# Kernel optimization log

Hardware: AMD Instinct MI355X
Metric: run time of the kernel (lower is better)

The kernel has to match this reference:

```python
import jax, jax.numpy as jnp
import numpy as np

D_MODEL = 1024
N_HEAD = 16
STRIDE = 1024
SEQ = STRIDE + 1  # time_mask is (stride+1, stride+1) -> N must equal stride+1
BATCH = 4
EPS = 1e-5


def layer_norm(x, g, b):
    mu = jnp.mean(x, axis=-1, keepdims=True)
    var = jnp.var(x, axis=-1, keepdims=True)
    return (x - mu) * jax.lax.rsqrt(var + EPS) * g + b


def quick_gelu(x):
    return x * jax.nn.sigmoid(1.702 * x)


def setup_inputs() -> dict:
    key = jax.random.key(0)
    ks = jax.random.split(key, 12)
    C = D_MODEL
    s = 0.02
    return {
        "x": jax.random.normal(ks[0], (SEQ, BATCH, C), dtype=jnp.float32),
        "qkv_w": jax.random.normal(ks[1], (3 * C, C), dtype=jnp.float32) * s,
        "proj_w": jax.random.normal(ks[2], (C, C), dtype=jnp.float32) * s,
        "proj_b": jnp.zeros((C,), dtype=jnp.float32),
        "ln1_g": jnp.ones((C,), dtype=jnp.float32),
        "ln1_b": jnp.zeros((C,), dtype=jnp.float32),
        "ln2_g": jnp.ones((C,), dtype=jnp.float32),
        "ln2_b": jnp.zeros((C,), dtype=jnp.float32),
        "fc_w": jax.random.normal(ks[3], (4 * C, C), dtype=jnp.float32) * s,
        "fc_b": jnp.zeros((4 * C,), dtype=jnp.float32),
        "cproj_w": jax.random.normal(ks[4], (C, 4 * C), dtype=jnp.float32) * s,
        "cproj_b": jnp.zeros((C,), dtype=jnp.float32),
    }


def _attention(xs, qkv_w, proj_w, proj_b):
    # xs: [N, B, C] (seq-first) -> internal [B, N, C]
    xb = jnp.transpose(xs, (1, 0, 2))
    B, N, C = xb.shape
    H, Dh = N_HEAD, C // N_HEAD
    scale = Dh ** -0.5
    qkv = xb @ qkv_w.T  # [B, N, 3C], no bias (qkv_bias=False)
    qkv = qkv.reshape(B, N, 3, H, Dh).transpose(2, 0, 3, 1, 4)  # [3, B, H, N, Dh]
    q, k, v = qkv[0], qkv[1], qkv[2]
    attn = jnp.einsum("bhnd,bhmd->bhnm", q, k) * scale
    mask = jnp.tril(jnp.ones((N, N), dtype=bool))  # time_mask: causal tril
    attn = jnp.where(mask, attn, -jnp.inf)
    attn = jax.nn.softmax(attn, axis=-1)
    out = jnp.einsum("bhnm,bhmd->bhnd", attn, v)  # [B, H, N, Dh]
    out = out.transpose(0, 2, 1, 3).reshape(B, N, C)
    out = out @ proj_w.T + proj_b
    return jnp.transpose(out, (1, 0, 2)), attn  # back to [N, B, C]


def reference(x, qkv_w, proj_w, proj_b, ln1_g, ln1_b, ln2_g, ln2_b,
              fc_w, fc_b, cproj_w, cproj_b):
    y, attn = _attention(layer_norm(x, ln1_g, ln1_b), qkv_w, proj_w, proj_b)
    x = x + y
    h = layer_norm(x, ln2_g, ln2_b)
    h = quick_gelu(h @ fc_w.T + fc_b) @ cproj_w.T + cproj_b
    x = x + h
    return (x, attn)
```

## Files before the change

### kernel.cpp

```cpp
#include <hip/hip_runtime.h>


typedef unsigned short ushort_t;
typedef __bf16 bf16x8 __attribute__((ext_vector_type(8)));
typedef float f32x4 __attribute__((ext_vector_type(4)));

#define SEQ_N   1025
#define CMODEL  1024
#define NHEAD   16
#define DH      64
#define TTOK    4100
#define MP      4224
#define NPAD    1152
#define BH      64

__device__ __forceinline__ ushort_t f2bf(float f) {
  union { float f; unsigned u; } v; v.f = f;
  unsigned r = v.u + 0x7fffu + ((v.u >> 16) & 1u);
  return (ushort_t)(r >> 16);
}

__device__ __forceinline__ void gl_lds16(const void* g, void* s) {
  __builtin_amdgcn_global_load_lds(
      (const __attribute__((address_space(1))) unsigned int*)g,
      (__attribute__((address_space(3))) unsigned int*)s, 16, 0, 0);
}

__global__ void cvt_bf(const float* __restrict__ src, ushort_t* __restrict__ dst, int n) {
  int i = (blockIdx.x * 256 + threadIdx.x) * 4;
  if (i >= n) return;
  float4 f = *(const float4*)(src + i);
  dst[i + 0] = f2bf(f.x);
  dst[i + 1] = f2bf(f.y);
  dst[i + 2] = f2bf(f.z);
  dst[i + 3] = f2bf(f.w);
}

__global__ __launch_bounds__(256)
void ln_bf(const float* __restrict__ xin, const float* __restrict__ g,
           const float* __restrict__ bb, ushort_t* __restrict__ out) {
  const int t = blockIdx.x;
  const float* row = xin + (size_t)t * CMODEL;
  const int base = threadIdx.x * 4;
  const float4 v = *(const float4*)(row + base);
  float s = v.x + v.y + v.z + v.w;
  float q = v.x * v.x + v.y * v.y + v.z * v.z + v.w * v.w;
#pragma unroll
  for (int off = 32; off > 0; off >>= 1) {
    s += __shfl_down(s, off);
    q += __shfl_down(q, off);
  }
  __shared__ float sh[8];
  const int wave = threadIdx.x >> 6, lane = threadIdx.x & 63;
  if (lane == 0) { sh[wave] = s; sh[4 + wave] = q; }
  __syncthreads();
  if (threadIdx.x == 0) {
    const float ts = sh[0] + sh[1] + sh[2] + sh[3];
    const float tq = sh[4] + sh[5] + sh[6] + sh[7];
    const float mean = ts * (1.f / CMODEL);
    const float var = tq * (1.f / CMODEL) - mean * mean;
    sh[0] = mean; sh[1] = rsqrtf(var + 1e-5f);
  }
  __syncthreads();
  const float mean = sh[0], rstd = sh[1];
  const float4 gg = *(const float4*)(g + base);
  const float4 bv = *(const float4*)(bb + base);
  ushort_t* orow = out + (size_t)t * CMODEL;
  orow[base + 0] = f2bf((v.x - mean) * rstd * gg.x + bv.x);
  orow[base + 1] = f2bf((v.y - mean) * rstd * gg.y + bv.y);
  orow[base + 2] = f2bf((v.z - mean) * rstd * gg.z + bv.z);
  orow[base + 3] = f2bf((v.w - mean) * rstd * gg.w + bv.w);
}

template <int EPI>
__global__ __launch_bounds__(256)
void gemm_bt(const ushort_t* __restrict__ A, int lda,
             const ushort_t* __restrict__ B, int ldb,
             int K,
             const float* __restrict__ bias, const float* __restrict__ res,
             float* __restrict__ outf, ushort_t* __restrict__ outb,
             ushort_t* __restrict__ oq, ushort_t* __restrict__ ok,
             ushort_t* __restrict__ ovt) {
  __shared__ __align__(16) ushort_t lsA[128 * 32];
  __shared__ __align__(16) ushort_t lsB[128 * 32];
  const int tid = threadIdx.x;
  const int wave = tid >> 6, lane = tid & 63;
  const int lr = lane & 15, quad = lane >> 4;
  const int tM = blockIdx.y * 128, tN = blockIdx.x * 128;
  const int waveM = (wave >> 1) * 64, waveN = (wave & 1) * 64;

  f32x4 acc[4][4];
  const f32x4 z4 = {0.f, 0.f, 0.f, 0.f};
#pragma unroll
  for (int i = 0; i < 4; ++i)
#pragma unroll
    for (int j = 0; j < 4; ++j) acc[i][j] = z4;

  for (int k0 = 0; k0 < K; k0 += 32) {
    __syncthreads();
#pragma unroll
    for (int p = 0; p < 2; ++p) {
      const int idx = p * 256 + wave * 64 + lane;
      const int row = idx >> 2, part = idx & 3;
      const int cb = (p * 256 + wave * 64) * 8;
      gl_lds16(A + (size_t)(tM + row) * lda + k0 + part * 8, lsA + cb);
      gl_lds16(B + (size_t)(tN + row) * ldb + k0 + part * 8, lsB + cb);
    }
    __syncthreads();
    bf16x8 af[4], bfr[4];
#pragma unroll
    for (int mi = 0; mi < 4; ++mi)
      af[mi] = *(const bf16x8*)(lsA + (waveM + mi * 16 + lr) * 32 + quad * 8);
#pragma unroll
    for (int ni = 0; ni < 4; ++ni)
      bfr[ni] = *(const bf16x8*)(lsB + (waveN + ni * 16 + lr) * 32 + quad * 8);
#pragma unroll
    for (int mi = 0; mi < 4; ++mi)
#pragma unroll
      for (int ni = 0; ni < 4; ++ni)
        acc[mi][ni] = __builtin_amdgcn_mfma_f32_16x16x32_bf16(af[mi], bfr[ni], acc[mi][ni], 0, 0, 0);
  }

#pragma unroll
  for (int mi = 0; mi < 4; ++mi) {
#pragma unroll
    for (int ni = 0; ni < 4; ++ni) {
#pragma unroll
      for (int r = 0; r < 4; ++r) {
        const int m = tM + waveM + mi * 16 + quad * 4 + r;
        const int n = tN + waveN + ni * 16 + lr;
        const float v = acc[mi][ni][r];
        if constexpr (EPI == 0) {
          if (m < TTOK) {
            const int b_ = m & 3, ns = m >> 2;
            const int which = n >> 10, rem = n & 1023, h = rem >> 6, d = rem & 63;
            const int bh = b_ * NHEAD + h;
            const ushort_t bv = f2bf(v);
            if (which == 0)      oq[((size_t)bh * NPAD + ns) * DH + d] = bv;
            else if (which == 1) ok[((size_t)bh * NPAD + ns) * DH + d] = bv;
            else                 ovt[((size_t)bh * DH + d) * NPAD + ns] = bv;
          }
        } else if constexpr (EPI == 3) {
          if (m < TTOK)
            outf[(size_t)m * CMODEL + n] = v + bias[n] + res[(size_t)m * CMODEL + n];
        } else if constexpr (EPI == 4) {
          if (m < TTOK) {
            const float zv = v + bias[n];
            outb[(size_t)m * 4096 + n] = f2bf(zv / (1.f + __expf(-1.702f * zv)));
          }
        }
      }
    }
  }
}

__global__ __launch_bounds__(256)
void attn_fused(const ushort_t* __restrict__ qb, const ushort_t* __restrict__ kb,
                const ushort_t* __restrict__ vtb, float* __restrict__ attn,
                ushort_t* __restrict__ ao) {
  __shared__ __align__(16) char smem[34816 + 17408 + 512];
  ushort_t* lsK  = (ushort_t*)smem;
  ushort_t* lsP  = (ushort_t*)smem;
  float*    lpart = (float*)smem;
  ushort_t* lsQV = (ushort_t*)(smem + 34816);
  float*    linvs = (float*)(smem + 34816 + 17408);

  const int bh = blockIdx.x;
  const int iT = 8 - blockIdx.y;
  const int tM = iT * 128;
  const int tid = threadIdx.x;
  const int wave = tid >> 6, lane = tid & 63;
  const int lr = lane & 15, quad = lane >> 4;
  const int waveM = (wave >> 1) * 64, waveN = (wave & 1) * 64;

  const ushort_t* Qg = qb + (size_t)bh * NPAD * DH;
  const ushort_t* Kg = kb + (size_t)bh * NPAD * DH;
  const ushort_t* Vg = vtb + (size_t)bh * DH * NPAD;
  float* attn_h = attn + (size_t)bh * ((size_t)SEQ_N * SEQ_N);

#pragma unroll
  for (int p = 0; p < 4; ++p) {
    const int c = p * 256 + wave * 64 + lane;
    const int ks = c >> 9, n = (c >> 2) & 127, part = c & 3;
    gl_lds16(Qg + (size_t)(tM + n) * DH + ks * 32 + part * 8,
             lsQV + (size_t)(p * 256 + wave * 64) * 8);
  }
  __syncthreads();
  bf16x8 aq[4][2];
#pragma unroll
  for (int mi = 0; mi < 4; ++mi)
#pragma unroll
    for (int ks = 0; ks < 2; ++ks)
      aq[mi][ks] = *(const bf16x8*)(lsQV + ks * 4096 + (waveM + mi * 16 + lr) * 32 + quad * 8);
  __syncthreads();

  f32x4 acc[4][4];
  const f32x4 z4 = {0.f, 0.f, 0.f, 0.f};

  float lsum[4][4];
#pragma unroll
  for (int mi = 0; mi < 4; ++mi)
#pragma unroll
    for (int r = 0; r < 4; ++r) lsum[mi][r] = 0.f;

  for (int j = 0; j <= iT; ++j) {
    __syncthreads();
#pragma unroll
    for (int p = 0; p < 4; ++p) {
      const int c = p * 256 + wave * 64 + lane;
      const int ks = c >> 9, n = (c >> 2) & 127, part = c & 3;
      gl_lds16(Kg + (size_t)(j * 128 + n) * DH + ks * 32 + part * 8,
               lsK + (size_t)(p * 256 + wave * 64) * 8);
    }
    __syncthreads();
#pragma unroll
    for (int mi = 0; mi < 4; ++mi)
#pragma unroll
      for (int ni = 0; ni < 4; ++ni) acc[mi][ni] = z4;
#pragma unroll
    for (int ks = 0; ks < 2; ++ks) {
      bf16x8 bk[4];
#pragma unroll
      for (int ni = 0; ni < 4; ++ni)
        bk[ni] = *(const bf16x8*)(lsK + ks * 4096 + (waveN + ni * 16 + lr) * 32 + quad * 8);
#pragma unroll
      for (int mi = 0; mi < 4; ++mi)
#pragma unroll
        for (int ni = 0; ni < 4; ++ni)
          acc[mi][ni] = __builtin_amdgcn_mfma_f32_16x16x32_bf16(aq[mi][ks], bk[ni], acc[mi][ni], 0, 0, 0);
    }
#pragma unroll
    for (int mi = 0; mi < 4; ++mi)
#pragma unroll
      for (int ni = 0; ni < 4; ++ni)
#pragma unroll
        for (int r = 0; r < 4; ++r) {
          const int row = tM + waveM + mi * 16 + quad * 4 + r;
          const int col = j * 128 + waveN + ni * 16 + lr;
          if (col <= row) lsum[mi][r] += __expf(acc[mi][ni][r] * 0.125f);
        }
  }
#pragma unroll
  for (int mi = 0; mi < 4; ++mi)
#pragma unroll
    for (int r = 0; r < 4; ++r) {
      float s = lsum[mi][r];
      s += __shfl_xor(s, 1); s += __shfl_xor(s, 2);
      s += __shfl_xor(s, 4); s += __shfl_xor(s, 8);
      lsum[mi][r] = s;
    }
  __syncthreads();
  if (lr == 0) {
    const int wx = wave & 1;
#pragma unroll
    for (int mi = 0; mi < 4; ++mi)
#pragma unroll
      for (int r = 0; r < 4; ++r)
        lpart[wx * 128 + waveM + mi * 16 + quad * 4 + r] = lsum[mi][r];
  }
  __syncthreads();
  if (tid < 128) linvs[tid] = 1.0f / (lpart[tid] + lpart[128 + tid]);
  __syncthreads();
  float linv[4][4];
#pragma unroll
  for (int mi = 0; mi < 4; ++mi)
#pragma unroll
    for (int r = 0; r < 4; ++r)
      linv[mi][r] = linvs[waveM + mi * 16 + quad * 4 + r];

  f32x4 oacc[2][4];
#pragma unroll
  for (int i = 0; i < 2; ++i)
#pragma unroll
    for (int j = 0; j < 4; ++j) oacc[i][j] = z4;
  const int prow = wave * 32;
  const int wrow = wave * 32;
  const int lcol = lane;

  for (int j = 0; j <= iT; ++j) {
    __syncthreads();
#pragma unroll
    for (int p = 0; p < 4; ++p) {
      const int c = p * 256 + wave * 64 + lane;
      const int ks = c >> 9, n = (c >> 2) & 127, part = c & 3;
      gl_lds16(Kg + (size_t)(j * 128 + n) * DH + ks * 32 + part * 8,
               lsK + (size_t)(p * 256 + wave * 64) * 8);
    }
#pragma unroll
    for (int p = 0; p < 4; ++p) {
      const int c = p * 256 + tid;
      const int n = c >> 4, klc = c & 15;
      const uint4 v = *(const uint4*)(Vg + (size_t)n * NPAD + j * 128 + klc * 8);
      *(uint4*)(lsQV + (size_t)n * 136 + klc * 8) = v;
    }
    __syncthreads();
#pragma unroll
    for (int mi = 0; mi < 4; ++mi)
#pragma unroll
      for (int ni = 0; ni < 4; ++ni) acc[mi][ni] = z4;
#pragma unroll
    for (int ks = 0; ks < 2; ++ks) {
      bf16x8 bk[4];
#pragma unroll
      for (int ni = 0; ni < 4; ++ni)
        bk[ni] = *(const bf16x8*)(lsK + ks * 4096 + (waveN + ni * 16 + lr) * 32 + quad * 8);
#pragma unroll
      for (int mi = 0; mi < 4; ++mi)
#pragma unroll
        for (int ni = 0; ni < 4; ++ni)
          acc[mi][ni] = __builtin_amdgcn_mfma_f32_16x16x32_bf16(aq[mi][ks], bk[ni], acc[mi][ni], 0, 0, 0);
    }
    __syncthreads();
#pragma unroll
    for (int mi = 0; mi < 4; ++mi)
#pragma unroll
      for (int ni = 0; ni < 4; ++ni)
#pragma unroll
        for (int r = 0; r < 4; ++r) {
          const int rowl = waveM + mi * 16 + quad * 4 + r;
          const int coll = waveN + ni * 16 + lr;
          const int row = tM + rowl;
          const int col = j * 128 + coll;
          const float pv = (col <= row) ? __expf(acc[mi][ni][r] * 0.125f) * linv[mi][r] : 0.f;
          lsP[(size_t)rowl * 136 + coll] = f2bf(pv);
        }
    __syncthreads();
#pragma unroll
    for (int ks = 0; ks < 4; ++ks) {
      bf16x8 ap[2], bv[4];
#pragma unroll
      for (int mi2 = 0; mi2 < 2; ++mi2)
        ap[mi2] = *(const bf16x8*)(lsP + (size_t)(prow + mi2 * 16 + lr) * 136 + ks * 32 + quad * 8);
#pragma unroll
      for (int ni = 0; ni < 4; ++ni)
        bv[ni] = *(const bf16x8*)(lsQV + (size_t)(ni * 16 + lr) * 136 + ks * 32 + quad * 8);
#pragma unroll
      for (int mi2 = 0; mi2 < 2; ++mi2)
#pragma unroll
        for (int ni = 0; ni < 4; ++ni)
          oacc[mi2][ni] = __builtin_amdgcn_mfma_f32_16x16x32_bf16(ap[mi2], bv[ni], oacc[mi2][ni], 0, 0, 0);
    }
#pragma unroll 8
    for (int rr = 0; rr < 32; ++rr) {
      const int grow = tM + wrow + rr;
      if (grow >= SEQ_N) break;
      const ushort_t* lrow = lsP + (size_t)(wrow + rr) * 136;
#pragma unroll
      for (int cb = 0; cb < 2; ++cb) {
        const int gcol = j * 128 + cb * 64 + lcol;
        union { unsigned u; float f; } cv;
        cv.u = ((unsigned)lrow[cb * 64 + lcol]) << 16;
        if (gcol < SEQ_N)
          __builtin_nontemporal_store(cv.f, attn_h + (size_t)grow * SEQ_N + gcol);
      }
    }
  }

  const int b_ = bh >> 4, h = bh & 15;
#pragma unroll
  for (int mi2 = 0; mi2 < 2; ++mi2)
#pragma unroll
    for (int ni = 0; ni < 4; ++ni)
#pragma unroll
      for (int r = 0; r < 4; ++r) {
        const int row = tM + prow + mi2 * 16 + quad * 4 + r;
        const int d = ni * 16 + lr;
        if (row < SEQ_N)
          ao[((size_t)row * 4 + b_) * CMODEL + h * DH + d] = f2bf(oacc[mi2][ni][r]);
      }

  const int c0 = tM + 128;
  if (c0 <= 1024) {
    const int width = 1025 - c0;
    for (int r = wave; r < 128; r += 4) {
      float* rp = attn_h + (size_t)(tM + r) * SEQ_N + c0;
      int pre = ((16 - (int)(((uintptr_t)rp) & 15)) >> 2) & 3;
      if (pre > width) pre = width;
      for (int c = lane; c < pre; c += 64) rp[c] = 0.f;
      const int body = (width - pre) >> 2;
      f32x4* bp = (f32x4*)(rp + pre);
      const f32x4 zf4 = {0.f, 0.f, 0.f, 0.f};
      for (int c = lane; c < body; c += 64) __builtin_nontemporal_store(zf4, bp + c);
      for (int c = pre + body * 4 + lane; c < width; c += 64) rp[c] = 0.f;
    }
  }
}

extern "C" void kernel_launch(void* const* d_in, const int* in_sizes, int n_in,
                              void* d_out, int out_size, void* d_ws, size_t ws_size,
                              hipStream_t stream) {
  const float* x       = (const float*)d_in[0];
  const float* qkv_w   = (const float*)d_in[1];
  const float* proj_w  = (const float*)d_in[2];
  const float* proj_b  = (const float*)d_in[3];
  const float* ln1_g   = (const float*)d_in[4];
  const float* ln1_b   = (const float*)d_in[5];
  const float* ln2_g   = (const float*)d_in[6];
  const float* ln2_b   = (const float*)d_in[7];
  const float* fc_w    = (const float*)d_in[8];
  const float* fc_b    = (const float*)d_in[9];
  const float* cproj_w = (const float*)d_in[10];
  const float* cproj_b = (const float*)d_in[11];

  float* out_x = (float*)d_out;
  float* out_attn = out_x + (size_t)TTOK * CMODEL;

  char* p = (char*)d_ws;
  auto alloc = [&](size_t bytes) { char* r = p; p += (bytes + 255) & ~(size_t)255; return r; };
  ushort_t* ln1x  = (ushort_t*)alloc((size_t)MP * CMODEL * 2);
  ushort_t* wqkv  = (ushort_t*)alloc((size_t)3072 * 1024 * 2);
  ushort_t* wproj = (ushort_t*)alloc((size_t)1024 * 1024 * 2);
  ushort_t* wfc   = (ushort_t*)alloc((size_t)4096 * 1024 * 2);
  ushort_t* wcpr  = (ushort_t*)alloc((size_t)1024 * 4096 * 2);
  ushort_t* qb    = (ushort_t*)alloc((size_t)BH * NPAD * DH * 2);
  ushort_t* kb    = (ushort_t*)alloc((size_t)BH * NPAD * DH * 2);
  ushort_t* vtb   = (ushort_t*)alloc((size_t)BH * DH * NPAD * 2);
  ushort_t* aob   = (ushort_t*)alloc((size_t)MP * CMODEL * 2);
  float*    x1    = (float*)alloc((size_t)MP * CMODEL * 4);
  ushort_t* ln2x  = (ushort_t*)alloc((size_t)MP * CMODEL * 2);
  ushort_t* hb    = (ushort_t*)alloc((size_t)MP * 4096 * 2);
  (void)ws_size; (void)in_sizes; (void)n_in; (void)out_size;

  cvt_bf<<<3072, 256, 0, stream>>>(qkv_w, wqkv, 3072 * 1024);
  cvt_bf<<<1024, 256, 0, stream>>>(proj_w, wproj, 1024 * 1024);
  cvt_bf<<<4096, 256, 0, stream>>>(fc_w, wfc, 4096 * 1024);
  cvt_bf<<<4096, 256, 0, stream>>>(cproj_w, wcpr, 4096 * 1024);

  ln_bf<<<TTOK, 256, 0, stream>>>(x, ln1_g, ln1_b, ln1x);

  gemm_bt<0><<<dim3(24, 33, 1), 256, 0, stream>>>(ln1x, 1024, wqkv, 1024, 1024,
      nullptr, nullptr, nullptr, nullptr, qb, kb, vtb);

  attn_fused<<<dim3(64, 9), 256, 0, stream>>>(qb, kb, vtb, out_attn, aob);

  gemm_bt<3><<<dim3(8, 33, 1), 256, 0, stream>>>(aob, 1024, wproj, 1024, 1024,
      proj_b, x, x1, nullptr, nullptr, nullptr, nullptr);

  ln_bf<<<TTOK, 256, 0, stream>>>(x1, ln2_g, ln2_b, ln2x);

  gemm_bt<4><<<dim3(32, 33, 1), 256, 0, stream>>>(ln2x, 1024, wfc, 1024, 1024,
      fc_b, nullptr, nullptr, hb, nullptr, nullptr, nullptr);

  gemm_bt<3><<<dim3(8, 33, 1), 256, 0, stream>>>(hb, 4096, wcpr, 4096, 4096,
      cproj_b, x1, out_x, nullptr, nullptr, nullptr, nullptr);
}
```

Before: 772.5 us.

## Split-K the N=1024 GEMMs with atomic accumulation onto LN-prefilled residuals

The projection and c_proj GEMMs, which launch only 8x33 tiles, now use split-K with two K halves along blockIdx.z and atomically add their partial results into the output. Each LayerNorm kernel pre-initialises that output with the residual plus the bias, so the GEMM epilogue no longer reads the residual. The four weight conversion launches are merged into one kernel, and s_setprio is raised around the MFMA sections of the attention kernel. The split doubles the number of blocks for these GEMMs, at the cost of fp32 atomics, a summation order that is no longer deterministic, and a dependency on the LN kernel having written the output first.

```diff
diff --git a/kernel.cpp b/kernel.cpp
--- a/kernel.cpp
+++ b/kernel.cpp
@@ -26,19 +26,29 @@
       (__attribute__((address_space(3))) unsigned int*)s, 16, 0, 0);
 }
 
-__global__ void cvt_bf(const float* __restrict__ src, ushort_t* __restrict__ dst, int n) {
-  int i = (blockIdx.x * 256 + threadIdx.x) * 4;
-  if (i >= n) return;
-  float4 f = *(const float4*)(src + i);
-  dst[i + 0] = f2bf(f.x);
-  dst[i + 1] = f2bf(f.y);
-  dst[i + 2] = f2bf(f.z);
-  dst[i + 3] = f2bf(f.w);
+__global__ __launch_bounds__(256)
+void cvt4(const float* __restrict__ s0, ushort_t* __restrict__ d0,
+          const float* __restrict__ s1, ushort_t* __restrict__ d1,
+          const float* __restrict__ s2, ushort_t* __restrict__ d2,
+          const float* __restrict__ s3, ushort_t* __restrict__ d3) {
+  const int b = blockIdx.x;
+  const float* s; ushort_t* d; int off;
+  if (b < 3072)      { s = s0; d = d0; off = b; }
+  else if (b < 4096) { s = s1; d = d1; off = b - 3072; }
+  else if (b < 8192) { s = s2; d = d2; off = b - 4096; }
+  else               { s = s3; d = d3; off = b - 8192; }
+  const int i = (off * 256 + threadIdx.x) * 4;
+  const float4 f = *(const float4*)(s + i);
+  d[i + 0] = f2bf(f.x);
+  d[i + 1] = f2bf(f.y);
+  d[i + 2] = f2bf(f.z);
+  d[i + 3] = f2bf(f.w);
 }
 
 __global__ __launch_bounds__(256)
 void ln_bf(const float* __restrict__ xin, const float* __restrict__ g,
-           const float* __restrict__ bb, ushort_t* __restrict__ out) {
+           const float* __restrict__ bb, ushort_t* __restrict__ out,
+           const float* __restrict__ rbias, float* __restrict__ resout) {
   const int t = blockIdx.x;
   const float* row = xin + (size_t)t * CMODEL;
   const int base = threadIdx.x * 4;
@@ -70,6 +80,12 @@
   orow[base + 1] = f2bf((v.y - mean) * rstd * gg.y + bv.y);
   orow[base + 2] = f2bf((v.z - mean) * rstd * gg.z + bv.z);
   orow[base + 3] = f2bf((v.w - mean) * rstd * gg.w + bv.w);
+  if (resout) {
+    const float4 rb = *(const float4*)(rbias + base);
+    float4 ro;
+    ro.x = v.x + rb.x; ro.y = v.y + rb.y; ro.z = v.z + rb.z; ro.w = v.w + rb.w;
+    *(float4*)(resout + (size_t)t * CMODEL + base) = ro;
+  }
 }
 
 template <int EPI>
@@ -87,6 +103,7 @@
   const int wave = tid >> 6, lane = tid & 63;
   const int lr = lane & 15, quad = lane >> 4;
   const int tM = blockIdx.y * 128, tN = blockIdx.x * 128;
+  const int kbase = blockIdx.z * K;
   const int waveM = (wave >> 1) * 64, waveN = (wave & 1) * 64;
 
   f32x4 acc[4][4];
@@ -103,8 +120,8 @@
       const int idx = p * 256 + wave * 64 + lane;
       const int row = idx >> 2, part = idx & 3;
       const int cb = (p * 256 + wave * 64) * 8;
-      gl_lds16(A + (size_t)(tM + row) * lda + k0 + part * 8, lsA + cb);
-      gl_lds16(B + (size_t)(tN + row) * ldb + k0 + part * 8, lsB + cb);
+      gl_lds16(A + (size_t)(tM + row) * lda + kbase + k0 + part * 8, lsA + cb);
+      gl_lds16(B + (size_t)(tN + row) * ldb + kbase + k0 + part * 8, lsB + cb);
     }
     __syncthreads();
     bf16x8 af[4], bfr[4];
@@ -148,6 +165,9 @@
             const float zv = v + bias[n];
             outb[(size_t)m * 4096 + n] = f2bf(zv / (1.f + __expf(-1.702f * zv)));
           }
+        } else if constexpr (EPI == 5) {
+          if (m < TTOK)
+            atomicAdd(outf + (size_t)m * CMODEL + n, v);
         }
       }
     }
@@ -217,6 +237,7 @@
     for (int mi = 0; mi < 4; ++mi)
 #pragma unroll
       for (int ni = 0; ni < 4; ++ni) acc[mi][ni] = z4;
+    __builtin_amdgcn_s_setprio(1);
 #pragma unroll
     for (int ks = 0; ks < 2; ++ks) {
       bf16x8 bk[4];
@@ -229,6 +250,7 @@
         for (int ni = 0; ni < 4; ++ni)
           acc[mi][ni] = __builtin_amdgcn_mfma_f32_16x16x32_bf16(aq[mi][ks], bk[ni], acc[mi][ni], 0, 0, 0);
     }
+    __builtin_amdgcn_s_setprio(0);
 #pragma unroll
     for (int mi = 0; mi < 4; ++mi)
 #pragma unroll
@@ -298,6 +320,7 @@
     for (int mi = 0; mi < 4; ++mi)
 #pragma unroll
       for (int ni = 0; ni < 4; ++ni) acc[mi][ni] = z4;
+    __builtin_amdgcn_s_setprio(1);
 #pragma unroll
     for (int ks = 0; ks < 2; ++ks) {
       bf16x8 bk[4];
@@ -310,6 +333,7 @@
         for (int ni = 0; ni < 4; ++ni)
           acc[mi][ni] = __builtin_amdgcn_mfma_f32_16x16x32_bf16(aq[mi][ks], bk[ni], acc[mi][ni], 0, 0, 0);
     }
+    __builtin_amdgcn_s_setprio(0);
     __syncthreads();
 #pragma unroll
     for (int mi = 0; mi < 4; ++mi)
@@ -325,6 +349,7 @@
           lsP[(size_t)rowl * 136 + coll] = f2bf(pv);
         }
     __syncthreads();
+    __builtin_amdgcn_s_setprio(1);
 #pragma unroll
     for (int ks = 0; ks < 4; ++ks) {
       bf16x8 ap[2], bv[4];
@@ -340,6 +365,7 @@
         for (int ni = 0; ni < 4; ++ni)
           oacc[mi2][ni] = __builtin_amdgcn_mfma_f32_16x16x32_bf16(ap[mi2], bv[ni], oacc[mi2][ni], 0, 0, 0);
     }
+    __builtin_amdgcn_s_setprio(0);
 #pragma unroll 8
     for (int rr = 0; rr < 32; ++rr) {
       const int grow = tM + wrow + rr;
@@ -421,26 +447,23 @@
   ushort_t* hb    = (ushort_t*)alloc((size_t)MP * 4096 * 2);
   (void)ws_size; (void)in_sizes; (void)n_in; (void)out_size;
 
-  cvt_bf<<<3072, 256, 0, stream>>>(qkv_w, wqkv, 3072 * 1024);
-  cvt_bf<<<1024, 256, 0, stream>>>(proj_w, wproj, 1024 * 1024);
-  cvt_bf<<<4096, 256, 0, stream>>>(fc_w, wfc, 4096 * 1024);
-  cvt_bf<<<4096, 256, 0, stream>>>(cproj_w, wcpr, 4096 * 1024);
-
-  ln_bf<<<TTOK, 256, 0, stream>>>(x, ln1_g, ln1_b, ln1x);
+  cvt4<<<12288, 256, 0, stream>>>(qkv_w, wqkv, proj_w, wproj, fc_w, wfc, cproj_w, wcpr);
+
+  ln_bf<<<TTOK, 256, 0, stream>>>(x, ln1_g, ln1_b, ln1x, proj_b, x1);
 
   gemm_bt<0><<<dim3(24, 33, 1), 256, 0, stream>>>(ln1x, 1024, wqkv, 1024, 1024,
       nullptr, nullptr, nullptr, nullptr, qb, kb, vtb);
 
   attn_fused<<<dim3(64, 9), 256, 0, stream>>>(qb, kb, vtb, out_attn, aob);
 
-  gemm_bt<3><<<dim3(8, 33, 1), 256, 0, stream>>>(aob, 1024, wproj, 1024, 1024,
-      proj_b, x, x1, nullptr, nullptr, nullptr, nullptr);
-
-  ln_bf<<<TTOK, 256, 0, stream>>>(x1, ln2_g, ln2_b, ln2x);
+  gemm_bt<5><<<dim3(8, 33, 2), 256, 0, stream>>>(aob, 1024, wproj, 1024, 512,
+      nullptr, nullptr, x1, nullptr, nullptr, nullptr, nullptr);
+
+  ln_bf<<<TTOK, 256, 0, stream>>>(x1, ln2_g, ln2_b, ln2x, cproj_b, out_x);
 
   gemm_bt<4><<<dim3(32, 33, 1), 256, 0, stream>>>(ln2x, 1024, wfc, 1024, 1024,
       fc_b, nullptr, nullptr, hb, nullptr, nullptr, nullptr);
 
-  gemm_bt<3><<<dim3(8, 33, 1), 256, 0, stream>>>(hb, 4096, wcpr, 4096, 4096,
-      cproj_b, x1, out_x, nullptr, nullptr, nullptr, nullptr);
-}
+  gemm_bt<5><<<dim3(8, 33, 2), 256, 0, stream>>>(hb, 4096, wcpr, 4096, 2048,
+      nullptr, nullptr, out_x, nullptr, nullptr, nullptr, nullptr);
+}
```

After: 745.6 us. 3.5% less time.
